# Kernel optimization log

Hardware: AMD Instinct MI355X
Metric: run time of the kernel (lower is better)

Reference implementation:

```python
import jax, jax.numpy as jnp
import numpy as np
from jax import lax

LRELU_SLOPE = 0.2
EPS = 1e-8


def eq_linear(x, W, b):
    # EqualizedLinear: weight scaled by 1/sqrt(fan_in)
    c = 1.0 / np.sqrt(W.shape[1])
    return x @ (W * c).T + b


def mod_conv(x, s, W, demod):
    # x: [b, cin, h, w], s: [b, cin], W: [cout, cin, k, k]
    b, cin, h, w = x.shape
    cout, _, k, _ = W.shape
    c = 1.0 / np.sqrt(cin * k * k)
    weights = (W * c)[None] * s[:, None, :, None, None]  # [b, cout, cin, k, k]
    if demod:
        sigma_inv = lax.rsqrt(jnp.sum(weights ** 2, axis=(2, 3, 4)) + EPS)  # [b, cout]
        weights = weights * sigma_inv[:, :, None, None, None]
    x2 = x.reshape(1, b * cin, h, w)
    wk = weights.reshape(b * cout, cin, k, k)
    pad = k // 2
    out = lax.conv_general_dilated(
        x2, wk, window_strides=(1, 1), padding=[(pad, pad), (pad, pad)],
        dimension_numbers=("NCHW", "OIHW", "NCHW"), feature_group_count=b)
    return out.reshape(b, cout, h, w)


def style_block(x, w, noise, style_W, style_b, conv_W, scale_noise, bias):
    A = eq_linear(w, style_W, style_b)          # [b, cin]
    x = mod_conv(x, A, conv_W, demod=True)      # [b, cout, h, w]
    if noise is not None:
        x = x + scale_noise[None, :, None, None] * noise
    return jax.nn.leaky_relu(x + bias[None, :, None, None], LRELU_SLOPE)


def rgb_block(x, w, style_W, style_b, conv_W, bias):
    A = eq_linear(w, style_W, style_b)
    x = mod_conv(x, A, conv_W, demod=False)     # 1x1 conv to 3 channels
    return jax.nn.leaky_relu(x + bias[None, :, None, None], LRELU_SLOPE)


def setup_inputs() -> dict:
    key = jax.random.key(0)
    ks = jax.random.split(key, 10)
    B, CIN, COUT, WD, H, W = 8, 512, 512, 512, 64, 64
    return {
        "x": jax.random.normal(ks[0], (B, CIN, H, W), jnp.float32),
        "w": jax.random.normal(ks[1], (B, WD), jnp.float32),
        "noise": jax.random.normal(ks[2], (2, B, 1, H, W), jnp.float32),
        # StyleBlock 1
        "s1_style_W": jax.random.normal(ks[3], (CIN, WD), jnp.float32),
        "s1_style_b": jnp.ones((CIN,), jnp.float32),
        "s1_conv_W": jax.random.normal(ks[4], (COUT, CIN, 3, 3), jnp.float32),
        "s1_scale_noise": jnp.zeros((1,), jnp.float32),
        "s1_bias": jnp.zeros((COUT,), jnp.float32),
        # StyleBlock 2
        "s2_style_W": jax.random.normal(ks[5], (COUT, WD), jnp.float32),
        "s2_style_b": jnp.ones((COUT,), jnp.float32),
        "s2_conv_W": jax.random.normal(ks[6], (COUT, COUT, 3, 3), jnp.float32),
        "s2_scale_noise": jnp.zeros((1,), jnp.float32),
        "s2_bias": jnp.zeros((COUT,), jnp.float32),
        # RGBBlock
        "rgb_style_W": jax.random.normal(ks[7], (COUT, WD), jnp.float32),
        "rgb_style_b": jnp.ones((COUT,), jnp.float32),
        "rgb_conv_W": jax.random.normal(ks[8], (3, COUT, 1, 1), jnp.float32),
        "rgb_bias": jnp.zeros((3,), jnp.float32),
    }


def reference(x, w, noise,
              s1_style_W, s1_style_b, s1_conv_W, s1_scale_noise, s1_bias,
              s2_style_W, s2_style_b, s2_conv_W, s2_scale_noise, s2_bias,
              rgb_style_W, rgb_style_b, rgb_conv_W, rgb_bias):
    x = style_block(x, w, noise[0], s1_style_W, s1_style_b, s1_conv_W, s1_scale_noise, s1_bias)
    x = style_block(x, w, noise[1], s2_style_W, s2_style_b, s2_conv_W, s2_scale_noise, s2_bias)
    rgb = rgb_block(x, w, rgb_style_W, rgb_style_b, rgb_conv_W, rgb_bias)
    return (x, rgb)
```

## Files before the change

kernel.cpp:

```cpp
#include <hip/hip_runtime.h>
#include <stdint.h>

typedef __attribute__((ext_vector_type(8))) short bf16x8;
typedef __attribute__((ext_vector_type(4))) float f32x4;

__device__ __forceinline__ ushort f2bf(float f) {
  uint32_t u = __builtin_bit_cast(uint32_t, f);
  u += 0x7fffu + ((u >> 16) & 1u);
  return (ushort)(u >> 16);
}

__device__ __forceinline__ void async_copy16(const void* gsrc, void* ldst) {
  __builtin_amdgcn_global_load_lds(
      (const __attribute__((address_space(1))) void*)gsrc,
      (__attribute__((address_space(3))) void*)ldst, 16, 0, 0);
}

__global__ void style_linear(const float* __restrict__ w, const float* __restrict__ sW,
                             const float* __restrict__ sb, float* __restrict__ A) {
  const int b = blockIdx.y;
  const int lane = threadIdx.x & 63, wv = threadIdx.x >> 6;
  const int co = blockIdx.x * 4 + wv;
  const float c = 0.04419417382415922f;
  const float* wr = w + b * 512;
  const float* Wr = sW + (size_t)co * 512;
  float s = 0.f;
#pragma unroll
  for (int i = 0; i < 8; ++i) {
    const int d = i * 64 + lane;
    s += wr[d] * Wr[d];
  }
#pragma unroll
  for (int off = 32; off; off >>= 1) s += __shfl_xor(s, off);
  if (lane == 0) A[b * 512 + co] = s * c + sb[co];
}

__global__ void prep_sigma(const float* __restrict__ Wc, const float* __restrict__ A,
                           ushort* __restrict__ Wt, float* __restrict__ sig) {
  const int co = blockIdx.x;
  const int ci = threadIdx.x;
  const int lane = ci & 63, wid = ci >> 6;
  const float c = 0.014731391274719738f;
  const float* src = Wc + ((size_t)co * 512 + ci) * 9;
  float s = 0.f;
#pragma unroll
  for (int t = 0; t < 9; ++t) {
    float v = src[t] * c;
    Wt[(size_t)t * 262144 + co * 512 + ci] = f2bf(v);
    s += v * v;
  }
  __shared__ float red[8][8];
#pragma unroll
  for (int b = 0; b < 8; ++b) {
    float a = A[b * 512 + ci];
    float v = s * a * a;
#pragma unroll
    for (int off = 32; off; off >>= 1) v += __shfl_xor(v, off);
    if (lane == 0) red[b][wid] = v;
  }
  __syncthreads();
  if (ci < 8) {
    float t = 0.f;
#pragma unroll
    for (int wv = 0; wv < 8; ++wv) t += red[ci][wv];
    sig[ci * 512 + co] = rsqrtf(t + 1e-8f);
  }
}

__global__ void zero_border(uint4* __restrict__ x1, uint4* __restrict__ x2,
                            uint4* __restrict__ rgb) {
  const int i = blockIdx.x * 256 + threadIdx.x;
  const int per = 16640;
  const int tot = per * 8;
  if (i >= 2 * tot) {
    const int j = i - 2 * tot;
    if (j < 24576) rgb[j] = make_uint4(0u, 0u, 0u, 0u);
    return;
  }
  uint4* base = (i < tot) ? x1 : x2;
  int t = (i < tot) ? i : i - tot;
  const int bb = t / per;
  int r = t - bb * per;
  int row, cell, q;
  if (r < 8448) {
    row = (r >= 4224) ? 65 : 0;
    int pos = (r >= 4224) ? r - 4224 : r;
    cell = pos >> 6;
    q = pos & 63;
  } else {
    int r2 = r - 8448;
    row = 1 + (r2 >> 7);
    cell = ((r2 >> 6) & 1) ? 65 : 0;
    q = r2 & 63;
  }
  base[(((size_t)bb * 66 + row) * 66 + cell) * 64 + q] = make_uint4(0u, 0u, 0u, 0u);
}

__global__ void mod_transpose(const float* __restrict__ X, const float* __restrict__ A,
                              ushort* __restrict__ xs) {
  __shared__ float tile[128][65];
  const int h = blockIdx.x;
  const int ci0 = blockIdx.y * 128;
  const int b = blockIdx.z;
  const int tid = threadIdx.x;
  const int wcol = tid & 63;
  const int r0 = tid >> 6;
#pragma unroll 4
  for (int i = 0; i < 32; ++i) {
    const int cil = r0 + i * 4;
    const int ci = ci0 + cil;
    const size_t off = ((size_t)(b * 512 + ci) * 64 + h) * 64 + wcol;
    tile[cil][wcol] = X[off] * A[b * 512 + ci];
  }
  __syncthreads();
  const int sub = tid & 3;
  const int w = tid >> 2;
  ushort* dst = xs + (((size_t)b * 66 + (h + 1)) * 66 + (w + 1)) * 512 + ci0 + sub * 32;
#pragma unroll
  for (int g = 0; g < 4; ++g) {
    bf16x8 v;
#pragma unroll
    for (int j = 0; j < 8; ++j) v[j] = (short)f2bf(tile[sub * 32 + g * 8 + j][w]);
    *(bf16x8*)(dst + g * 8) = v;
  }
}

#define WAITVM(N) __builtin_amdgcn_s_waitcnt(0x0F70 | (N))

#define READS(S, AF, BV)                                                     \
  do {                                                                       \
    const int q_ = (S) & 3;                                                  \
    const char* baA = (const char*)(&smA[0][0] + q_ * 8192);                 \
    const char* baB = (const char*)(&smB[0][0] + q_ * 8192);                 \
    _Pragma("unroll") for (int m_ = 0; m_ < 8; ++m_)                         \
        AF[m_] = *(const bf16x8*)(baA + aro[m_]);                            \
    _Pragma("unroll") for (int n_ = 0; n_ < 4; ++n_)                         \
        BV[n_] = *(const bf16x8*)(baB + bro[n_]);                            \
  } while (0)

#define PH(S, WN, DOREAD, DOSTAGE, RAF, RBV, MAF, MBV)                               \
  do {                                                                               \
    WAITVM(WN);                                                                      \
    __builtin_amdgcn_s_barrier();                                                    \
    __builtin_amdgcn_sched_barrier(0);                                               \
    if (DOREAD) READS((S) + 1, RAF, RBV);                                            \
    if (DOSTAGE) stage((S) + 3);                                                     \
    __builtin_amdgcn_sched_barrier(0);                                               \
    __builtin_amdgcn_s_setprio(1);                                                   \
    _Pragma("unroll") for (int m_ = 0; m_ < 8; ++m_)                                 \
      _Pragma("unroll") for (int n_ = 0; n_ < 4; ++n_)                               \
        acc[m_][n_] = __builtin_amdgcn_mfma_f32_16x16x32_bf16(MAF[m_], MBV[n_],      \
                                                              acc[m_][n_], 0, 0, 0); \
    __builtin_amdgcn_s_setprio(0);                                                   \
    __builtin_amdgcn_sched_barrier(0);                                               \
  } while (0)

template <int OUT_MODE>
__global__ __launch_bounds__(512, 2) void conv3x3(
    const ushort* __restrict__ xs, const ushort* __restrict__ Wt,
    const float* __restrict__ sig, const float* __restrict__ noise,
    const float* __restrict__ scale_noise, const float* __restrict__ bias,
    const float* __restrict__ amod, void* __restrict__ outp,
    const float* __restrict__ rgbw, const float* __restrict__ arr,
    float* __restrict__ outrgb) {
  __shared__ __align__(16) ushort smA[4][8192];
  __shared__ __align__(16) ushort smB[4][8192];
  const int tid = threadIdx.x, lane = tid & 63, wid = tid >> 6;
  const int wr = wid >> 2, wc = wid & 3;
  const int id = blockIdx.x;
  const int b = id & 7;
  const int tile = id >> 3;
  const int co0 = (tile & 1) * 256;
  const int px0 = (tile >> 1) * 256;
  const int h0 = px0 >> 6;

  const int sswz = ((lane & 3) ^ ((lane >> 3) & 3)) * 8;
  int aoff[2], boff[2];
  ushort *ldsA[2], *ldsB[2];
#pragma unroll
  for (int i = 0; i < 2; ++i) {
    const int row = (i * 8 + wid) * 16 + (lane >> 2);
    aoff[i] = (co0 + row) * 512 + sswz;
    const int hh = h0 + (row >> 6), ww = row & 63;
    boff[i] = ((b * 66 + hh) * 66 + ww) * 512 + sswz;
    ldsA[i] = &smA[0][0] + (i * 8 + wid) * 512 + lane * 8;
    ldsB[i] = &smB[0][0] + (i * 8 + wid) * 512 + lane * 8;
  }
  const int rdsw = ((lane >> 4) ^ ((lane >> 1) & 3)) * 16;
  int aro[8], bro[4];
#pragma unroll
  for (int m = 0; m < 8; ++m) aro[m] = (wr * 128 + m * 16 + (lane & 15)) * 64 + rdsw;
#pragma unroll
  for (int n = 0; n < 4; ++n) bro[n] = (wc * 64 + n * 16 + (lane & 15)) * 64 + rdsw;

  f32x4 acc[8][4];
#pragma unroll
  for (int m = 0; m < 8; ++m)
#pragma unroll
    for (int n = 0; n < 4; ++n) acc[m][n] = (f32x4){0.f, 0.f, 0.f, 0.f};

  auto stage = [&](int s) {
    const int tap = s >> 4;
    const int ci0 = (s & 15) << 5;
    const int kh = tap / 3;
    const int kw = tap - kh * 3;
    const int q = s & 3;
    const ushort* Wb = Wt + tap * 262144 + ci0;
    const ushort* Xb = xs + (kh * 66 + kw) * 512 + ci0;
    async_copy16(Wb + aoff[0], ldsA[0] + q * 8192);
    async_copy16(Wb + aoff[1], ldsA[1] + q * 8192);
    async_copy16(Xb + boff[0], ldsB[0] + q * 8192);
    async_copy16(Xb + boff[1], ldsB[1] + q * 8192);
  };

  bf16x8 afA[8], bvA[4], afB[8], bvB[4];

  stage(0);
  stage(1);
  stage(2);
  WAITVM(8);
  __builtin_amdgcn_s_barrier();
  __builtin_amdgcn_sched_barrier(0);
  READS(0, afA, bvA);

  for (int s = 0; s < 140; s += 2) {
    PH(s, 4, true, true, afB, bvB, afA, bvA);
    PH(s + 1, 4, true, true, afA, bvA, afB, bvB);
  }
  PH(140, 4, true, true, afB, bvB, afA, bvA);
  PH(141, 4, true, false, afA, bvA, afB, bvB);
  PH(142, 0, true, false, afB, bvB, afA, bvA);
  PH(143, 0, false, false, afA, bvA, afB, bvB);

  const float sn = scale_noise[0];
  const int colp = lane & 15;
  const int rq = (lane >> 4) * 4;
  float nz[4];
#pragma unroll
  for (int n = 0; n < 4; ++n)
    nz[n] = sn * noise[b * 4096 + px0 + wc * 64 + n * 16 + colp];
  float rgbp[3][4];
#pragma unroll
  for (int c = 0; c < 3; ++c)
#pragma unroll
    for (int n = 0; n < 4; ++n) rgbp[c][n] = 0.f;
#pragma unroll
  for (int m = 0; m < 8; ++m) {
    const int cob = co0 + wr * 128 + m * 16 + rq;
    float sg[4], bs[4], am[4];
    float w0[4], w1[4], w2[4];
#pragma unroll
    for (int r = 0; r < 4; ++r) {
      sg[r] = sig[b * 512 + cob + r];
      bs[r] = bias[cob + r];
      if (OUT_MODE == 0) {
        am[r] = amod[b * 512 + cob + r];
      } else {
        const float a3 = arr[b * 512 + cob + r] * 0.04419417382415922f;
        w0[r] = rgbw[cob + r] * a3;
        w1[r] = rgbw[512 + cob + r] * a3;
        w2[r] = rgbw[1024 + cob + r] * a3;
      }
    }
#pragma unroll
    for (int n = 0; n < 4; ++n) {
      const int px = px0 + wc * 64 + n * 16 + colp;
      if (OUT_MODE == 0) {
        const int hh = px >> 6, ww = px & 63;
        ushort pk[4];
#pragma unroll
        for (int r = 0; r < 4; ++r) {
          float v = acc[m][n][r] * sg[r] + nz[n] + bs[r];
          v = (v > 0.f) ? v : 0.2f * v;
          pk[r] = f2bf(v * am[r]);
        }
        uint2 u;
        u.x = (uint32_t)pk[0] | ((uint32_t)pk[1] << 16);
        u.y = (uint32_t)pk[2] | ((uint32_t)pk[3] << 16);
        *(uint2*)((ushort*)outp + (((size_t)b * 66 + hh + 1) * 66 + (ww + 1)) * 512 + cob) = u;
      } else {
#pragma unroll
        for (int r = 0; r < 4; ++r) {
          float v = acc[m][n][r] * sg[r] + nz[n] + bs[r];
          v = (v > 0.f) ? v : 0.2f * v;
          ((float*)outp)[((size_t)b * 512 + cob + r) * 4096 + px] = v;
          rgbp[0][n] += w0[r] * v;
          rgbp[1][n] += w1[r] * v;
          rgbp[2][n] += w2[r] * v;
        }
      }
    }
  }
  if (OUT_MODE == 1) {
#pragma unroll
    for (int c = 0; c < 3; ++c)
#pragma unroll
      for (int n = 0; n < 4; ++n) {
        float s = rgbp[c][n];
        s += __shfl_xor(s, 16);
        s += __shfl_xor(s, 32);
        if (lane < 16)
          atomicAdd(&outrgb[((size_t)b * 3 + c) * 4096 + px0 + wc * 64 + n * 16 + colp], s);
      }
  }
}

__global__ void rgb_finish(float* __restrict__ o, const float* __restrict__ rb) {
  const int i = blockIdx.x * 256 + threadIdx.x;
  if (i >= 98304) return;
  const int c = (i >> 12) % 3;
  float v = o[i] + rb[c];
  o[i] = (v > 0.f) ? v : 0.2f * v;
}

extern "C" void kernel_launch(void* const* d_in, const int* in_sizes, int n_in,
                              void* d_out, int out_size, void* d_ws, size_t ws_size,
                              hipStream_t stream) {
  const float* x     = (const float*)d_in[0];
  const float* w     = (const float*)d_in[1];
  const float* noise = (const float*)d_in[2];
  const float* s1_sW = (const float*)d_in[3];
  const float* s1_sb = (const float*)d_in[4];
  const float* s1_cW = (const float*)d_in[5];
  const float* s1_sn = (const float*)d_in[6];
  const float* s1_b  = (const float*)d_in[7];
  const float* s2_sW = (const float*)d_in[8];
  const float* s2_sb = (const float*)d_in[9];
  const float* s2_cW = (const float*)d_in[10];
  const float* s2_sn = (const float*)d_in[11];
  const float* s2_b  = (const float*)d_in[12];
  const float* r_sW  = (const float*)d_in[13];
  const float* r_sb  = (const float*)d_in[14];
  const float* r_cW  = (const float*)d_in[15];
  const float* r_b   = (const float*)d_in[16];

  char* ws = (char*)d_ws;
  float*  A1  = (float*)(ws + 0);
  float*  A2  = (float*)(ws + 16384);
  float*  Arr = (float*)(ws + 32768);
  float*  sg1 = (float*)(ws + 49152);
  float*  sg2 = (float*)(ws + 65536);
  ushort* Wt1 = (ushort*)(ws + 98304);
  ushort* xs1 = (ushort*)(ws + 4816896);
  ushort* Wt2 = (ushort*)(ws + 4816896);
  ushort* xs2 = (ushort*)(ws + 40501248);
  float* outx   = (float*)d_out;
  float* outrgb = outx + (size_t)8 * 512 * 4096;

  style_linear<<<dim3(128, 8), 256, 0, stream>>>(w, s1_sW, s1_sb, A1);
  style_linear<<<dim3(128, 8), 256, 0, stream>>>(w, s2_sW, s2_sb, A2);
  style_linear<<<dim3(128, 8), 256, 0, stream>>>(w, r_sW, r_sb, Arr);

  prep_sigma<<<512, 512, 0, stream>>>(s1_cW, A1, Wt1, sg1);

  zero_border<<<1136, 256, 0, stream>>>((uint4*)xs1, (uint4*)xs2, (uint4*)outrgb);
  mod_transpose<<<dim3(64, 4, 8), 256, 0, stream>>>(x, A1, xs1);

  conv3x3<0><<<dim3(256), 512, 0, stream>>>(xs1, Wt1, sg1, noise, s1_sn, s1_b, A2, (void*)xs2,
                                            r_cW, Arr, outrgb);
  prep_sigma<<<512, 512, 0, stream>>>(s2_cW, A2, Wt2, sg2);
  conv3x3<1><<<dim3(256), 512, 0, stream>>>(xs2, Wt2, sg2, noise + 32768, s2_sn, s2_b, sg2,
                                            (void*)outx, r_cW, Arr, outrgb);
  rgb_finish<<<384, 256, 0, stream>>>(outrgb, r_b);
}
```

Baseline: 322.5 us.

## Split conv main loop into two half-MFMA phases with single fragment set

The K-loop of the implicit-GEMM conv is restructured so that each stage runs as two phases. Each phase reads half of the A fragments (plus the B fragments in the first), issues half of the async global-to-LDS copies, and runs 16 MFMAs. Register double-buffering of fragments is dropped in favour of a single af/bv set, and the copy prefetch distance falls from three stages ahead to two. This is meant to cut VGPR pressure and interleave LDS reads with MFMAs more finely. In exchange it adds more barriers per stage and leaves less latency hiding for global loads.

Result: slower. 390.5 us (+21.1%).

```diff
diff --git a/kernel.cpp b/kernel.cpp
--- a/kernel.cpp
+++ b/kernel.cpp
@@ -126,33 +126,49 @@
 }
 
 #define WAITVM(N) __builtin_amdgcn_s_waitcnt(0x0F70 | (N))
-
-#define READS(S, AF, BV)                                                     \
-  do {                                                                       \
-    const int q_ = (S) & 3;                                                  \
-    const char* baA = (const char*)(&smA[0][0] + q_ * 8192);                 \
-    const char* baB = (const char*)(&smB[0][0] + q_ * 8192);                 \
-    _Pragma("unroll") for (int m_ = 0; m_ < 8; ++m_)                         \
-        AF[m_] = *(const bf16x8*)(baA + aro[m_]);                            \
-    _Pragma("unroll") for (int n_ = 0; n_ < 4; ++n_)                         \
-        BV[n_] = *(const bf16x8*)(baB + bro[n_]);                            \
+#define WAITLGKM0 __builtin_amdgcn_s_waitcnt(0xC07F)
+
+#define PH1(S, DOSTAGE)                                                              \
+  do {                                                                               \
+    const int q_ = (S) & 3;                                                          \
+    const char* baA = (const char*)(&smA[0][0] + q_ * 8192);                         \
+    const char* baB = (const char*)(&smB[0][0] + q_ * 8192);                         \
+    _Pragma("unroll") for (int m_ = 0; m_ < 4; ++m_)                                 \
+        af[m_] = *(const bf16x8*)(baA + aro[m_]);                                    \
+    _Pragma("unroll") for (int n_ = 0; n_ < 4; ++n_)                                 \
+        bv[n_] = *(const bf16x8*)(baB + bro[n_]);                                    \
+    if (DOSTAGE) stage_a((S) + 2);                                                   \
+    __builtin_amdgcn_s_barrier();                                                    \
+    WAITLGKM0;                                                                       \
+    __builtin_amdgcn_sched_barrier(0);                                               \
+    __builtin_amdgcn_s_setprio(1);                                                   \
+    _Pragma("unroll") for (int m_ = 0; m_ < 4; ++m_)                                 \
+      _Pragma("unroll") for (int n_ = 0; n_ < 4; ++n_)                               \
+        acc[m_][n_] = __builtin_amdgcn_mfma_f32_16x16x32_bf16(af[m_], bv[n_],        \
+                                                              acc[m_][n_], 0, 0, 0); \
+    __builtin_amdgcn_s_setprio(0);                                                   \
+    __builtin_amdgcn_s_barrier();                                                    \
   } while (0)
 
-#define PH(S, WN, DOREAD, DOSTAGE, RAF, RBV, MAF, MBV)                               \
+#define PH2(S, WN, DOSTAGE)                                                          \
   do {                                                                               \
+    const int q_ = (S) & 3;                                                          \
+    const char* baA = (const char*)(&smA[0][0] + q_ * 8192);                         \
+    _Pragma("unroll") for (int m_ = 0; m_ < 4; ++m_)                                 \
+        af[4 + m_] = *(const bf16x8*)(baA + aro[4 + m_]);                            \
+    if (DOSTAGE) stage_b((S) + 2);                                                   \
     WAITVM(WN);                                                                      \
     __builtin_amdgcn_s_barrier();                                                    \
-    __builtin_amdgcn_sched_barrier(0);                                               \
-    if (DOREAD) READS((S) + 1, RAF, RBV);                                            \
-    if (DOSTAGE) stage((S) + 3);                                                     \
+    WAITLGKM0;                                                                       \
     __builtin_amdgcn_sched_barrier(0);                                               \
     __builtin_amdgcn_s_setprio(1);                                                   \
-    _Pragma("unroll") for (int m_ = 0; m_ < 8; ++m_)                                 \
+    _Pragma("unroll") for (int m_ = 0; m_ < 4; ++m_)                                 \
       _Pragma("unroll") for (int n_ = 0; n_ < 4; ++n_)                               \
-        acc[m_][n_] = __builtin_amdgcn_mfma_f32_16x16x32_bf16(MAF[m_], MBV[n_],      \
-                                                              acc[m_][n_], 0, 0, 0); \
+        acc[4 + m_][n_] = __builtin_amdgcn_mfma_f32_16x16x32_bf16(af[4 + m_], bv[n_],\
+                                                                  acc[4 + m_][n_],  \
+                                                                  0, 0, 0);          \
     __builtin_amdgcn_s_setprio(0);                                                   \
-    __builtin_amdgcn_sched_barrier(0);                                               \
+    __builtin_amdgcn_s_barrier();                                                    \
   } while (0)
 
 template <int OUT_MODE>
@@ -199,38 +215,42 @@
 #pragma unroll
     for (int n = 0; n < 4; ++n) acc[m][n] = (f32x4){0.f, 0.f, 0.f, 0.f};
 
-  auto stage = [&](int s) {
+  auto stage_a = [&](int s) {
+    const int tap = s >> 4;
+    const int ci0 = (s & 15) << 5;
+    const int q = s & 3;
+    const ushort* Wb = Wt + tap * 262144 + ci0;
+    async_copy16(Wb + aoff[0], ldsA[0] + q * 8192);
+    async_copy16(Wb + aoff[1], ldsA[1] + q * 8192);
+  };
+  auto stage_b = [&](int s) {
     const int tap = s >> 4;
     const int ci0 = (s & 15) << 5;
     const int kh = tap / 3;
     const int kw = tap - kh * 3;
     const int q = s & 3;
-    const ushort* Wb = Wt + tap * 262144 + ci0;
     const ushort* Xb = xs + (kh * 66 + kw) * 512 + ci0;
-    async_copy16(Wb + aoff[0], ldsA[0] + q * 8192);
-    async_copy16(Wb + aoff[1], ldsA[1] + q * 8192);
     async_copy16(Xb + boff[0], ldsB[0] + q * 8192);
     async_copy16(Xb + boff[1], ldsB[1] + q * 8192);
   };
 
-  bf16x8 afA[8], bvA[4], afB[8], bvB[4];
-
-  stage(0);
-  stage(1);
-  stage(2);
-  WAITVM(8);
+  bf16x8 af[8], bv[4];
+
+  stage_a(0);
+  stage_b(0);
+  stage_a(1);
+  stage_b(1);
+  WAITVM(4);
   __builtin_amdgcn_s_barrier();
-  __builtin_amdgcn_sched_barrier(0);
-  READS(0, afA, bvA);
-
-  for (int s = 0; s < 140; s += 2) {
-    PH(s, 4, true, true, afB, bvB, afA, bvA);
-    PH(s + 1, 4, true, true, afA, bvA, afB, bvB);
-  }
-  PH(140, 4, true, true, afB, bvB, afA, bvA);
-  PH(141, 4, true, false, afA, bvA, afB, bvB);
-  PH(142, 0, true, false, afB, bvB, afA, bvA);
-  PH(143, 0, false, false, afA, bvA, afB, bvB);
+
+  for (int s = 0; s < 142; ++s) {
+    PH1(s, true);
+    PH2(s, 4, true);
+  }
+  PH1(142, false);
+  PH2(142, 0, false);
+  PH1(143, false);
+  PH2(143, 0, false);
 
   const float sn = scale_noise[0];
   const int colp = lane & 15;
```
